# Kernel tuning notes

Hardware: AMD Instinct MI355X
Metric: run time of the kernel (lower is better)

Reference implementation:

```python
import jax, jax.numpy as jnp
import numpy as np

THRESH = 0.5
POOL_K = 8  # feature_hw // proto_grid = 128 // 16
EPS = 1e-4
NEG = -1e30


def _avg_pool(x, k):
    # x: [n, c, h, w] -> [n, c, h//k, w//k]
    n, c, h, w = x.shape
    return x.reshape(n, c, h // k, k, w // k, k).mean(axis=(3, 5))


def reference(qry, sup_x, sup_y):
    # squeeze as in forward
    qry = qry[:, 0]          # [B=1, C, H, W]
    sup_x = sup_x[0, :, 0]   # [shot, C, H, W]
    sup_y = sup_y[0]         # [shot, 1, H, W]

    shot, nch, H, W = sup_x.shape

    # grid prototypes via avg pooling
    n_sup = _avg_pool(sup_x, POOL_K)                      # [shot, C, gh, gw]
    y_g = _avg_pool(sup_y, POOL_K)                        # [shot, 1, gh, gw]

    cand = n_sup.reshape(shot, nch, -1).transpose(0, 2, 1).reshape(-1, nch)  # [M, C]
    y_flat = y_g.reshape(-1)                              # [M]

    # threshold mask with fallback chain (thresh -> 0.1 -> all), static shapes
    m1 = y_flat > THRESH
    m2 = y_flat > 0.1
    m_all = jnp.ones_like(m1)
    mask = jnp.where(jnp.any(m1), m1, jnp.where(jnp.any(m2), m2, m_all))  # [M]

    # mean-center and safe L2-normalize prototypes (per proto over channels)
    protos = cand - cand.mean(axis=-1, keepdims=True)
    pro_n = protos / jnp.maximum(jnp.linalg.norm(protos, axis=1, keepdims=True), EPS)  # [M, C]

    # mean-center and safe L2-normalize query (per pixel over channels)
    qc = qry - qry.mean(axis=1, keepdims=True)
    qry_n = qc / jnp.maximum(jnp.linalg.norm(qc, axis=1, keepdims=True), EPS)          # [B, C, H, W]

    # cosine-sim 1x1 conv = GEMM, scaled
    dists = jnp.einsum('bchw,mc->bmhw', qry_n, pro_n) * 20.0                           # [B, M, H, W]

    # masked softmax over prototypes (equivalent to selecting masked subset)
    logits = jnp.where(mask[None, :, None, None], dists, NEG)
    prob = jax.nn.softmax(logits, axis=1)                                              # [B, M, H, W]

    # weighted back-projection and final similarity map
    ch_proto = jnp.einsum('mc,bmhw->bchw', pro_n, prob)                                # [B, C, H, W]
    pred_grid = jnp.sum(qry_n * ch_proto * 20.0, axis=1, keepdims=True)                # [B, 1, H, W]
    return pred_grid


def setup_inputs() -> dict:
    key = jax.random.key(0)
    k1, k2, k3 = jax.random.split(key, 3)
    qry = jax.random.normal(k1, (1, 1, 256, 128, 128), dtype=jnp.float32)
    sup_x = jax.random.normal(k2, (1, 5, 1, 256, 128, 128), dtype=jnp.float32)
    sup_y = jax.random.uniform(k3, (1, 5, 1, 128, 128), dtype=jnp.float32)
    return {"qry": qry, "sup_x": sup_x, "sup_y": sup_y}
```

## Files before the change

### kernel.cpp

```cpp
#include <hip/hip_runtime.h>
#include <math.h>

typedef _Float16 f16x8 __attribute__((ext_vector_type(8)));
typedef float f32x4 __attribute__((ext_vector_type(4)));


__global__ __launch_bounds__(256) void pool_kernel(const float* __restrict__ sup_x,
                                                   const float* __restrict__ sup_y,
                                                   float* __restrict__ cand_T,
                                                   float* __restrict__ yv_ws) {
    const int b = blockIdx.x, t = threadIdx.x;
    if (b < 1280) {
        __shared__ float hs[4096];
        const int s = b >> 8, c = b & 255;
        const float4* plane = (const float4*)(sup_x + (size_t)(s * 256 + c) * 16384);
#pragma unroll
        for (int it = 0; it < 16; ++it) {
            const float4 v = plane[it * 256 + t];
            hs[it * 256 + t] = v.x + v.y + v.z + v.w;
        }
        __syncthreads();
        const int gy = t >> 4, gx = t & 15;
        float sum = 0.f;
#pragma unroll
        for (int rr = 0; rr < 8; ++rr)
            sum += hs[(gy * 8 + rr) * 32 + 2 * gx] + hs[(gy * 8 + rr) * 32 + 2 * gx + 1];
        cand_T[(size_t)c * 1280 + s * 256 + t] = sum * (1.f / 64.f);
    } else {
        const int r = b - 1280;
        const int gy = t >> 4, gx = t & 15;
        const float* base = sup_y + r * 16384 + gy * 1024 + gx * 8;
        float sum = 0.f;
#pragma unroll
        for (int rr = 0; rr < 8; ++rr) {
            const float4 a = *(const float4*)(base + rr * 128);
            const float4 bb = *(const float4*)(base + rr * 128 + 4);
            sum += a.x + a.y + a.z + a.w + bb.x + bb.y + bb.z + bb.w;
        }
        yv_ws[r * 256 + t] = sum * (1.f / 64.f);
    }
}

__global__ __launch_bounds__(256) void fin_kernel(const float* __restrict__ cand_T,
                                                  const float* __restrict__ yv_ws,
                                                  _Float16* __restrict__ pro_h,
                                                  float* __restrict__ maskf) {
    const int b = blockIdx.x, t = threadIdx.x;
    if (b < 20) {
        __shared__ float tile[256 * 65];
        __shared__ float scr[640];
        const int m0 = b * 64;
        for (int it = 0; it < 64; ++it) {
            const int idx = it * 256 + t;
            tile[(idx >> 6) * 65 + (idx & 63)] =
                cand_T[(size_t)(idx >> 6) * 1280 + m0 + (idx & 63)];
        }
        __syncthreads();
        {
            const int ml = t & 63, part = t >> 6;
            float s1 = 0.f, s2 = 0.f;
            for (int cc = 0; cc < 64; ++cc) {
                const float x = tile[(part * 64 + cc) * 65 + ml];
                s1 += x; s2 += x * x;
            }
            scr[part * 64 + ml] = s1; scr[256 + part * 64 + ml] = s2;
        }
        __syncthreads();
        if (t < 64) {
            float S1 = 0.f, S2 = 0.f;
            for (int p = 0; p < 4; ++p) { S1 += scr[p * 64 + t]; S2 += scr[256 + p * 64 + t]; }
            const float mu = S1 * (1.f / 256.f);
            const float nrm = sqrtf(fmaxf(S2 - 256.f * mu * mu, 0.f));
            scr[512 + t] = mu; scr[576 + t] = 1.f / fmaxf(nrm, 1e-4f);
        }
        __syncthreads();
        const int ml = t >> 2, q = t & 3;
        const float mu = scr[512 + ml], inv = scr[576 + ml];
#pragma unroll
        for (int u = 0; u < 8; ++u) {
            const int g = u * 4 + q;
            f16x8 hv;
#pragma unroll
            for (int j = 0; j < 8; ++j)
                hv[j] = (_Float16)((tile[(g * 8 + j) * 65 + ml] - mu) * inv);
            *(f16x8*)(pro_h + (size_t)(m0 + ml) * 256 + ((g ^ (ml & 7)) << 3)) = hv;
        }
    } else {
        __shared__ int flags[2];
        if (t < 2) flags[t] = 0;
        __syncthreads();
        float yloc[5];
#pragma unroll
        for (int it = 0; it < 5; ++it) {
            const float y = yv_ws[it * 256 + t];
            yloc[it] = y;
            if (y > 0.5f) atomicOr(&flags[0], 1);
            if (y > 0.1f) atomicOr(&flags[1], 1);
        }
        __syncthreads();
        const int mode = flags[0] ? 0 : (flags[1] ? 1 : 2);
#pragma unroll
        for (int it = 0; it < 5; ++it) {
            const float y = yloc[it];
            maskf[it * 256 + t] = (mode == 0) ? (y > 0.5f ? 1.f : 0.f)
                                : (mode == 1) ? (y > 0.1f ? 1.f : 0.f) : 1.f;
        }
    }
}

__device__ __forceinline__ void gload_lds16h(const _Float16* g, _Float16* l) {
    __builtin_amdgcn_global_load_lds((const __attribute__((address_space(1))) unsigned int*)g,
                                     (__attribute__((address_space(3))) unsigned int*)l,
                                     16, 0, 0);
}
__device__ __forceinline__ void gload_lds16f(const float* g, float* l) {
    __builtin_amdgcn_global_load_lds((const __attribute__((address_space(1))) unsigned int*)g,
                                     (__attribute__((address_space(3))) unsigned int*)l,
                                     16, 0, 0);
}

__device__ __forceinline__ void stage_tile(const _Float16* __restrict__ pro_h,
                                           int tile, _Float16* dst, int w, int l) {
#pragma unroll
    for (int i = 0; i < 8; ++i) {
        const int off = w * 4096 + i * 512 + l * 8;
        gload_lds16h(pro_h + (size_t)tile * 32768 + off, dst + off);
    }
}

__device__ __forceinline__ void compute_tile(const _Float16* __restrict__ pb,
                                             const float* __restrict__ msp,
                                             const f16x8 (&bfr)[4][8],
                                             int row, int ln7, int lq,
                                             float (&Sa)[4], float (&Wa)[4]) {
    f32x4 acc[4];
#pragma unroll
    for (int p = 0; p < 4; ++p) acc[p] = (f32x4){0.f, 0.f, 0.f, 0.f};
#pragma unroll
    for (int ks = 0; ks < 8; ++ks) {
        const int ch = (ks * 4 + lq) ^ ln7;
        const f16x8 a = *(const f16x8*)(pb + row * 256 + ch * 8);
#pragma unroll
        for (int p = 0; p < 4; ++p)
            acc[p] = __builtin_amdgcn_mfma_f32_16x16x32_f16(a, bfr[p][ks], acc[p], 0, 0, 0);
    }
    const f32x4 mkv = *(const f32x4*)(msp + lq * 4);
#pragma unroll
    for (int p = 0; p < 4; ++p) {
        float ssum = 0.f, wsum = 0.f;
#pragma unroll
        for (int r = 0; r < 4; ++r) {
            const float d = 20.f * acc[p][r];
            const float e = mkv[r] * __expf(d - 20.f);
            ssum += e; wsum += e * d;
        }
        Sa[p] += ssum; Wa[p] += wsum;
    }
}

__global__ __launch_bounds__(512, 2) void main_kernel(const float* __restrict__ qry,
                                                      const _Float16* __restrict__ pro_h,
                                                      const float* __restrict__ maskf,
                                                      float* __restrict__ out) {
    __shared__ __align__(16) _Float16 arena[65536];
    __shared__ float ms[1280];
    __shared__ float scr[1024];
    __shared__ float2 stats[64];

    float*     qtf  = (float*)arena;
    _Float16*  qs   = arena + 32768;
    _Float16*  buf0 = arena;
    _Float16*  buf1 = arena + 32768;
    float*     red  = (float*)arena;

    const int t = threadIdx.x;
    const int w = t >> 6, l = t & 63;
    const int ln = l & 15, lq = l >> 4;
    const int ln7 = ln & 7;
    const int px0 = blockIdx.x * 64;

#pragma unroll
    for (int i = 0; i < 8; ++i) {
        const int c = i * 32 + (t >> 4);
        gload_lds16f(qry + (size_t)c * 16384 + px0 + (t & 15) * 4,
                     qtf + i * 2048 + t * 4);
    }
#pragma unroll
    for (int it = 0; it < 3; ++it) {
        const int idx = it * 512 + t;
        if (idx < 1280) ms[idx] = maskf[idx];
    }
    __syncthreads();
    {
        const int p = t & 63, q = t >> 6;
        float s1 = 0.f, s2 = 0.f;
        for (int cc = 0; cc < 32; ++cc) {
            const float x = qtf[(q * 32 + cc) * 64 + p];
            s1 += x; s2 += x * x;
        }
        scr[q * 64 + p] = s1; scr[512 + q * 64 + p] = s2;
    }
    __syncthreads();
    if (t < 64) {
        float S1 = 0.f, S2 = 0.f;
        for (int q = 0; q < 8; ++q) { S1 += scr[q * 64 + t]; S2 += scr[512 + q * 64 + t]; }
        const float mu = S1 * (1.f / 256.f);
        const float nrm = sqrtf(fmaxf(S2 - 256.f * mu * mu, 0.f));
        stats[t] = make_float2(mu, 1.f / fmaxf(nrm, 1e-4f));
    }
    __syncthreads();
    {
        const int px = t & 63, e = t >> 6;
        const float2 st = stats[px];
#pragma unroll
        for (int u = 0; u < 4; ++u) {
            const int g = e * 4 + u;
            f16x8 hv;
#pragma unroll
            for (int j = 0; j < 8; ++j)
                hv[j] = (_Float16)((qtf[(g * 8 + j) * 64 + px] - st.x) * st.y);
            *(f16x8*)(qs + px * 256 + ((g ^ (px & 7)) << 3)) = hv;
        }
    }
    __syncthreads();

    f16x8 bfr[4][8];
#pragma unroll
    for (int p = 0; p < 4; ++p) {
        const int px = p * 16 + ln;
        const int sB = px & 7;
#pragma unroll
        for (int ks = 0; ks < 8; ++ks) {
            const int g = ks * 4 + lq;
            bfr[p][ks] = *(const f16x8*)(qs + px * 256 + ((g ^ sB) << 3));
        }
    }
    __syncthreads();

    stage_tile(pro_h, 0, buf0, w, l);
    stage_tile(pro_h, 1, buf1, w, l);

    const int row = w * 16 + ln;
    float Sa[4] = {0.f, 0.f, 0.f, 0.f}, Wa[4] = {0.f, 0.f, 0.f, 0.f};

#pragma unroll 1
    for (int tile = 0; tile < 10; ++tile) {
        if (tile < 8) asm volatile("s_waitcnt vmcnt(8)" ::: "memory");
        else          asm volatile("s_waitcnt vmcnt(0)" ::: "memory");
        compute_tile((tile & 1) ? buf1 : buf0, ms + tile * 128 + w * 16,
                     bfr, row, ln7, lq, Sa, Wa);
        if (tile < 8) {
            asm volatile("s_waitcnt lgkmcnt(0)" ::: "memory");
            __builtin_amdgcn_sched_barrier(0);
            stage_tile(pro_h, tile + 2, (tile & 1) ? buf1 : buf0, w, l);
        }
    }

    __syncthreads();
#pragma unroll
    for (int p = 0; p < 4; ++p) {
        const int px = p * 16 + ln;
        const int slot = (w * 4 + lq + px) & 31;
        red[px * 32 + slot] = Sa[p];
        red[2048 + px * 32 + slot] = Wa[p];
    }
    __syncthreads();
    if (t < 64) {
        float S = 0.f, W = 0.f;
        for (int s = 0; s < 32; ++s) {
            const int slot = (s + t) & 31;
            S += red[t * 32 + slot];
            W += red[2048 + t * 32 + slot];
        }
        out[px0 + t] = W / S;
    }
}

extern "C" void kernel_launch(void* const* d_in, const int* in_sizes, int n_in,
                              void* d_out, int out_size, void* d_ws, size_t ws_size,
                              hipStream_t stream) {
    const float* qry   = (const float*)d_in[0];
    const float* sup_x = (const float*)d_in[1];
    const float* sup_y = (const float*)d_in[2];
    float* out = (float*)d_out;

    char* ws = (char*)d_ws;
    float*     cand_T = (float*)ws;               ws += 256 * 1280 * 4;
    float*     yv_ws  = (float*)ws;               ws += 1280 * 4;
    float*     maskf  = (float*)ws;               ws += 1280 * 4;
    _Float16*  pro_h  = (_Float16*)ws;

    pool_kernel<<<1285, 256, 0, stream>>>(sup_x, sup_y, cand_T, yv_ws);
    fin_kernel<<<21, 256, 0, stream>>>(cand_T, yv_ws, pro_h, maskf);
    main_kernel<<<256, 512, 0, stream>>>(qry, pro_h, maskf, out);
}
```

Before: 41.99 us.

## Fold prototype normalization into per-prototype GEMM scale and drop the finalize kernel

Pooled prototypes are now written straight from the pool kernel as raw fp16 rows in swizzled layout, together with per-channel-group partial sums and sums of squares. Centering is dropped because the query is already mean-centered, so the dot product with a raw prototype matches the centered one. L2 normalization becomes a per-prototype scale alpha applied to the MFMA result. The threshold mask and alpha are recomputed in every main-kernel block, which removes the fin_kernel launch and the fp32 cand_T round trip through memory. In exchange, each of the 256 blocks redundantly reads the psum and yv arrays, and raw uncentered values are rounded to fp16.

```diff
diff --git a/kernel.cpp b/kernel.cpp
--- a/kernel.cpp
+++ b/kernel.cpp
@@ -7,27 +7,54 @@
 
 __global__ __launch_bounds__(256) void pool_kernel(const float* __restrict__ sup_x,
                                                    const float* __restrict__ sup_y,
-                                                   float* __restrict__ cand_T,
+                                                   _Float16* __restrict__ pro_raw,
+                                                   float* __restrict__ psum,
                                                    float* __restrict__ yv_ws) {
     const int b = blockIdx.x, t = threadIdx.x;
-    if (b < 1280) {
-        __shared__ float hs[4096];
-        const int s = b >> 8, c = b & 255;
-        const float4* plane = (const float4*)(sup_x + (size_t)(s * 256 + c) * 16384);
-#pragma unroll
-        for (int it = 0; it < 16; ++it) {
-            const float4 v = plane[it * 256 + t];
-            hs[it * 256 + t] = v.x + v.y + v.z + v.w;
+    if (b < 640) {
+        __shared__ float hs[8192];
+        __shared__ float xa[16][33];
+        const int s = b >> 7, rem = b & 127;
+        const int gy = rem >> 3, cq = rem & 7;
+        const float* base = sup_x + ((size_t)(s * 256 + cq * 32) * 128 + gy * 8) * 128;
+#pragma unroll 8
+        for (int i = 0; i < 32; ++i) {
+            const int run = i * 8 + (t >> 5);
+            const float4 v = *(const float4*)(base + ((size_t)(run >> 3) * 128 + (run & 7)) * 128 + (t & 31) * 4);
+            hs[i * 256 + t] = v.x + v.y + v.z + v.w;
         }
         __syncthreads();
-        const int gy = t >> 4, gx = t & 15;
-        float sum = 0.f;
-#pragma unroll
-        for (int rr = 0; rr < 8; ++rr)
-            sum += hs[(gy * 8 + rr) * 32 + 2 * gx] + hs[(gy * 8 + rr) * 32 + 2 * gx + 1];
-        cand_T[(size_t)c * 1280 + s * 256 + t] = sum * (1.f / 64.f);
+#pragma unroll
+        for (int e0 = 0; e0 < 2; ++e0) {
+            const int e = e0 * 256 + t;
+            const int c = e >> 4, gx = e & 15;
+            float sum = 0.f;
+#pragma unroll
+            for (int r = 0; r < 8; ++r)
+                sum += hs[(c * 8 + r) * 32 + gx * 2] + hs[(c * 8 + r) * 32 + gx * 2 + 1];
+            xa[gx][c] = sum * (1.f / 64.f);
+        }
+        __syncthreads();
+        const int mbase = s * 256 + gy * 16;
+        if (t < 64) {
+            const int gx = t >> 2, gi = t & 3;
+            const int m = mbase + gx;
+            const int g = cq * 4 + gi;
+            f16x8 hv;
+#pragma unroll
+            for (int j = 0; j < 8; ++j) hv[j] = (_Float16)xa[gx][gi * 8 + j];
+            *(f16x8*)(pro_raw + (size_t)m * 256 + ((g ^ (m & 7)) << 3)) = hv;
+        } else if (t < 80) {
+            const int gx = t - 64;
+            float s1 = 0.f, s2 = 0.f;
+#pragma unroll
+            for (int c = 0; c < 32; ++c) { const float x = xa[gx][c]; s1 += x; s2 += x * x; }
+            const int m = mbase + gx;
+            psum[m * 16 + cq * 2]     = s1;
+            psum[m * 16 + cq * 2 + 1] = s2;
+        }
     } else {
-        const int r = b - 1280;
+        const int r = b - 640;
         const int gy = t >> 4, gx = t & 15;
         const float* base = sup_y + r * 16384 + gy * 1024 + gx * 8;
         float sum = 0.f;
@@ -41,73 +68,6 @@
     }
 }
 
-__global__ __launch_bounds__(256) void fin_kernel(const float* __restrict__ cand_T,
-                                                  const float* __restrict__ yv_ws,
-                                                  _Float16* __restrict__ pro_h,
-                                                  float* __restrict__ maskf) {
-    const int b = blockIdx.x, t = threadIdx.x;
-    if (b < 20) {
-        __shared__ float tile[256 * 65];
-        __shared__ float scr[640];
-        const int m0 = b * 64;
-        for (int it = 0; it < 64; ++it) {
-            const int idx = it * 256 + t;
-            tile[(idx >> 6) * 65 + (idx & 63)] =
-                cand_T[(size_t)(idx >> 6) * 1280 + m0 + (idx & 63)];
-        }
-        __syncthreads();
-        {
-            const int ml = t & 63, part = t >> 6;
-            float s1 = 0.f, s2 = 0.f;
-            for (int cc = 0; cc < 64; ++cc) {
-                const float x = tile[(part * 64 + cc) * 65 + ml];
-                s1 += x; s2 += x * x;
-            }
-            scr[part * 64 + ml] = s1; scr[256 + part * 64 + ml] = s2;
-        }
-        __syncthreads();
-        if (t < 64) {
-            float S1 = 0.f, S2 = 0.f;
-            for (int p = 0; p < 4; ++p) { S1 += scr[p * 64 + t]; S2 += scr[256 + p * 64 + t]; }
-            const float mu = S1 * (1.f / 256.f);
-            const float nrm = sqrtf(fmaxf(S2 - 256.f * mu * mu, 0.f));
-            scr[512 + t] = mu; scr[576 + t] = 1.f / fmaxf(nrm, 1e-4f);
-        }
-        __syncthreads();
-        const int ml = t >> 2, q = t & 3;
-        const float mu = scr[512 + ml], inv = scr[576 + ml];
-#pragma unroll
-        for (int u = 0; u < 8; ++u) {
-            const int g = u * 4 + q;
-            f16x8 hv;
-#pragma unroll
-            for (int j = 0; j < 8; ++j)
-                hv[j] = (_Float16)((tile[(g * 8 + j) * 65 + ml] - mu) * inv);
-            *(f16x8*)(pro_h + (size_t)(m0 + ml) * 256 + ((g ^ (ml & 7)) << 3)) = hv;
-        }
-    } else {
-        __shared__ int flags[2];
-        if (t < 2) flags[t] = 0;
-        __syncthreads();
-        float yloc[5];
-#pragma unroll
-        for (int it = 0; it < 5; ++it) {
-            const float y = yv_ws[it * 256 + t];
-            yloc[it] = y;
-            if (y > 0.5f) atomicOr(&flags[0], 1);
-            if (y > 0.1f) atomicOr(&flags[1], 1);
-        }
-        __syncthreads();
-        const int mode = flags[0] ? 0 : (flags[1] ? 1 : 2);
-#pragma unroll
-        for (int it = 0; it < 5; ++it) {
-            const float y = yloc[it];
-            maskf[it * 256 + t] = (mode == 0) ? (y > 0.5f ? 1.f : 0.f)
-                                : (mode == 1) ? (y > 0.1f ? 1.f : 0.f) : 1.f;
-        }
-    }
-}
-
 __device__ __forceinline__ void gload_lds16h(const _Float16* g, _Float16* l) {
     __builtin_amdgcn_global_load_lds((const __attribute__((address_space(1))) unsigned int*)g,
                                      (__attribute__((address_space(3))) unsigned int*)l,
@@ -119,17 +79,18 @@
                                      16, 0, 0);
 }
 
-__device__ __forceinline__ void stage_tile(const _Float16* __restrict__ pro_h,
+__device__ __forceinline__ void stage_tile(const _Float16* __restrict__ pro_raw,
                                            int tile, _Float16* dst, int w, int l) {
 #pragma unroll
     for (int i = 0; i < 8; ++i) {
         const int off = w * 4096 + i * 512 + l * 8;
-        gload_lds16h(pro_h + (size_t)tile * 32768 + off, dst + off);
+        gload_lds16h(pro_raw + (size_t)tile * 32768 + off, dst + off);
     }
 }
 
 __device__ __forceinline__ void compute_tile(const _Float16* __restrict__ pb,
                                              const float* __restrict__ msp,
+                                             const float* __restrict__ asp,
                                              const f16x8 (&bfr)[4][8],
                                              int row, int ln7, int lq,
                                              float (&Sa)[4], float (&Wa)[4]) {
@@ -145,12 +106,13 @@
             acc[p] = __builtin_amdgcn_mfma_f32_16x16x32_f16(a, bfr[p][ks], acc[p], 0, 0, 0);
     }
     const f32x4 mkv = *(const f32x4*)(msp + lq * 4);
+    const f32x4 av  = *(const f32x4*)(asp + lq * 4);
 #pragma unroll
     for (int p = 0; p < 4; ++p) {
         float ssum = 0.f, wsum = 0.f;
 #pragma unroll
         for (int r = 0; r < 4; ++r) {
-            const float d = 20.f * acc[p][r];
+            const float d = av[r] * acc[p][r];
             const float e = mkv[r] * __expf(d - 20.f);
             ssum += e; wsum += e * d;
         }
@@ -159,13 +121,16 @@
 }
 
 __global__ __launch_bounds__(512, 2) void main_kernel(const float* __restrict__ qry,
-                                                      const _Float16* __restrict__ pro_h,
-                                                      const float* __restrict__ maskf,
+                                                      const _Float16* __restrict__ pro_raw,
+                                                      const float* __restrict__ psum,
+                                                      const float* __restrict__ yv_ws,
                                                       float* __restrict__ out) {
     __shared__ __align__(16) _Float16 arena[65536];
     __shared__ float ms[1280];
+    __shared__ float alf[1280];
     __shared__ float scr[1024];
     __shared__ float2 stats[64];
+    __shared__ int iflags[2];
 
     float*     qtf  = (float*)arena;
     _Float16*  qs   = arena + 32768;
@@ -179,18 +144,49 @@
     const int ln7 = ln & 7;
     const int px0 = blockIdx.x * 64;
 
+    if (t < 2) iflags[t] = 0;
+    __syncthreads();
+
 #pragma unroll
     for (int i = 0; i < 8; ++i) {
         const int c = i * 32 + (t >> 4);
         gload_lds16f(qry + (size_t)c * 16384 + px0 + (t & 15) * 4,
                      qtf + i * 2048 + t * 4);
     }
-#pragma unroll
-    for (int it = 0; it < 3; ++it) {
-        const int idx = it * 512 + t;
-        if (idx < 1280) ms[idx] = maskf[idx];
-    }
-    __syncthreads();
+
+    float yv3[3];
+    int f0 = 0, f1 = 0;
+#pragma unroll
+    for (int k = 0; k < 3; ++k) {
+        const int m = t + k * 512;
+        if (m < 1280) {
+            const f32x4 p0 = *(const f32x4*)(psum + m * 16);
+            const f32x4 p1 = *(const f32x4*)(psum + m * 16 + 4);
+            const f32x4 p2 = *(const f32x4*)(psum + m * 16 + 8);
+            const f32x4 p3 = *(const f32x4*)(psum + m * 16 + 12);
+            const float S1 = p0[0] + p0[2] + p1[0] + p1[2] + p2[0] + p2[2] + p3[0] + p3[2];
+            const float S2 = p0[1] + p0[3] + p1[1] + p1[3] + p2[1] + p2[3] + p3[1] + p3[3];
+            alf[m] = 20.f / fmaxf(sqrtf(fmaxf(S2 - S1 * S1 * (1.f / 256.f), 0.f)), 1e-4f);
+            const float y = yv_ws[m];
+            yv3[k] = y;
+            if (y > 0.5f) f0 = 1;
+            if (y > 0.1f) f1 = 1;
+        }
+    }
+    if (f0) atomicOr(&iflags[0], 1);
+    if (f1) atomicOr(&iflags[1], 1);
+    __syncthreads();
+    {
+        const int mode = iflags[0] ? 0 : (iflags[1] ? 1 : 2);
+#pragma unroll
+        for (int k = 0; k < 3; ++k) {
+            const int m = t + k * 512;
+            if (m < 1280)
+                ms[m] = (mode == 0) ? (yv3[k] > 0.5f ? 1.f : 0.f)
+                      : (mode == 1) ? (yv3[k] > 0.1f ? 1.f : 0.f) : 1.f;
+        }
+    }
+
     {
         const int p = t & 63, q = t >> 6;
         float s1 = 0.f, s2 = 0.f;
@@ -224,6 +220,8 @@
     }
     __syncthreads();
 
+    stage_tile(pro_raw, 0, buf0, w, l);
+
     f16x8 bfr[4][8];
 #pragma unroll
     for (int p = 0; p < 4; ++p) {
@@ -237,8 +235,7 @@
     }
     __syncthreads();
 
-    stage_tile(pro_h, 0, buf0, w, l);
-    stage_tile(pro_h, 1, buf1, w, l);
+    stage_tile(pro_raw, 1, buf1, w, l);
 
     const int row = w * 16 + ln;
     float Sa[4] = {0.f, 0.f, 0.f, 0.f}, Wa[4] = {0.f, 0.f, 0.f, 0.f};
@@ -247,12 +244,13 @@
     for (int tile = 0; tile < 10; ++tile) {
         if (tile < 8) asm volatile("s_waitcnt vmcnt(8)" ::: "memory");
         else          asm volatile("s_waitcnt vmcnt(0)" ::: "memory");
-        compute_tile((tile & 1) ? buf1 : buf0, ms + tile * 128 + w * 16,
+        compute_tile((tile & 1) ? buf1 : buf0,
+                     ms + tile * 128 + w * 16, alf + tile * 128 + w * 16,
                      bfr, row, ln7, lq, Sa, Wa);
         if (tile < 8) {
             asm volatile("s_waitcnt lgkmcnt(0)" ::: "memory");
             __builtin_amdgcn_sched_barrier(0);
-            stage_tile(pro_h, tile + 2, (tile & 1) ? buf1 : buf0, w, l);
+            stage_tile(pro_raw, tile + 2, (tile & 1) ? buf1 : buf0, w, l);
         }
     }
 
@@ -285,12 +283,10 @@
     float* out = (float*)d_out;
 
     char* ws = (char*)d_ws;
-    float*     cand_T = (float*)ws;               ws += 256 * 1280 * 4;
-    float*     yv_ws  = (float*)ws;               ws += 1280 * 4;
-    float*     maskf  = (float*)ws;               ws += 1280 * 4;
-    _Float16*  pro_h  = (_Float16*)ws;
-
-    pool_kernel<<<1285, 256, 0, stream>>>(sup_x, sup_y, cand_T, yv_ws);
-    fin_kernel<<<21, 256, 0, stream>>>(cand_T, yv_ws, pro_h, maskf);
-    main_kernel<<<256, 512, 0, stream>>>(qry, pro_h, maskf, out);
-}
+    _Float16*  pro_raw = (_Float16*)ws;           ws += 1280 * 256 * 2;
+    float*     psum    = (float*)ws;              ws += 1280 * 16 * 4;
+    float*     yv_ws   = (float*)ws;
+
+    pool_kernel<<<645, 256, 0, stream>>>(sup_x, sup_y, pro_raw, psum, yv_ws);
+    main_kernel<<<256, 512, 0, stream>>>(qry, pro_raw, psum, yv_ws, out);
+}
```

New measurement: 39.43 us. 1.06x faster.
